# Performance work log

Measured on AMD Instinct MI355X. Metric: run time of the kernel, lower is better.

## Reference

```python
import jax, jax.numpy as jnp
from jax import lax
import numpy as np

GB_MAX = 3      # BandEst guard-band upper bound
RB = 1          # refer_band
PAD = RB + 1    # refer_band + init_guard_band(1)
N_OFF = 16      # ring offsets: kernel (4,4) -> N=16
BN_EPS = 1e-5

def _ring_offsets():
    idx = np.arange(-PAD, PAD + 1)
    X, Y = np.meshgrid(idx, idx, indexing='ij')
    hp = wp = 2 * PAD + 1
    def ring(M):
        return np.concatenate([M[0:RB, 0:wp - RB].ravel(), M[0:hp - RB, wp - RB:wp].ravel(),
                               M[hp - RB:hp, RB:wp].ravel(), M[RB:hp, 0:RB].ravel()])
    return ring(X).astype(np.float32), ring(Y).astype(np.float32)

PRF_X, PRF_Y = _ring_offsets()
BLOCK = np.repeat(np.arange(4), N_OFF // 4)  # offset n -> direction block (top,right,bottom,left)


def q_shift(x, H, W, shift=1, gamma=0.25):
    B, T, C = x.shape
    img = x.transpose(0, 2, 1).reshape(B, C, H, W)
    g = int(C * gamma)
    out = jnp.zeros_like(img)
    out = out.at[:, 0:g, :, shift:].set(img[:, 0:g, :, :W - shift])
    out = out.at[:, g:2 * g, :, :W - shift].set(img[:, g:2 * g, :, shift:])
    out = out.at[:, 2 * g:3 * g, shift:, :].set(img[:, 2 * g:3 * g, :H - shift, :])
    out = out.at[:, 3 * g:4 * g, :H - shift, :].set(img[:, 3 * g:4 * g, shift:, :])
    out = out.at[:, 4 * g:].set(img[:, 4 * g:])
    return out.reshape(B, C, T).transpose(0, 2, 1)


def bi_wkv(w, u, k, v):
    # Bi-directional WKV: y_t = (sum_{i<t} e^{-(t-1-i)w + k_i} v_i + e^{u+k_t} v_t
    #                            + sum_{i>t} e^{-(i-1-t)w + k_i} v_i) / (same with v->1)
    B, T, C = k.shape
    kT = k.transpose(1, 0, 2)
    vT = v.transpose(1, 0, 2)

    def step(carry, kv):
        m, a, b = carry  # state represents e^m * (a, b): (sum exp, weighted v)
        kt, vt = kv
        out = (m, a, b)  # exclusive prefix (excludes current token)
        m2 = jnp.maximum(m - w, kt)
        e1 = jnp.exp(m - w - m2)
        e2 = jnp.exp(kt - m2)
        return (m2, e1 * a + e2, e1 * b + e2 * vt), out

    init = (jnp.full((B, C), -1e38, k.dtype), jnp.zeros((B, C), k.dtype), jnp.zeros((B, C), k.dtype))
    _, (mf, af, bf) = lax.scan(step, init, (kT, vT))
    _, (mb, ab, bb) = lax.scan(step, init, (kT[::-1], vT[::-1]))
    mb, ab, bb = mb[::-1], ab[::-1], bb[::-1]
    ms = u + kT
    M = jnp.maximum(jnp.maximum(mf, mb), ms)
    ef, eb, es = jnp.exp(mf - M), jnp.exp(mb - M), jnp.exp(ms - M)
    num = ef * bf + eb * bb + es * vT
    den = ef * af + eb * ab + es
    return (num / den).transpose(1, 0, 2)


def band_est(x, cvw, cvb, bns_v, bnb_v, chw, chb, bns_h, bnb_h):
    dn = ('NCHW', 'OIHW', 'NCHW')
    gv = lax.conv_general_dilated(x, cvw, (1, 1), ((GB_MAX, GB_MAX), (0, 0)), dimension_numbers=dn) + cvb[None, :, None, None]
    gh = lax.conv_general_dilated(x, chw, (1, 1), ((0, 0), (GB_MAX, GB_MAX)), dimension_numbers=dn) + chb[None, :, None, None]
    inv = np.float32(1.0 / np.sqrt(1.0 + BN_EPS))  # eval BN: running mean 0, var 1
    gv = gv * (bns_v * inv)[None, :, None, None] + bnb_v[None, :, None, None]
    gh = gh * (bns_h * inv)[None, :, None, None] + bnb_h[None, :, None, None]
    return jnp.concatenate([jax.nn.sigmoid(gv), jax.nn.sigmoid(gh)], 1) * (GB_MAX - 1)


def _gather(xp_flat, ix, iy, wp, h, w):
    b, c = xp_flat.shape[0], xp_flat.shape[1]
    idx = (ix * wp + iy).reshape(b, 1, -1)
    return jnp.take_along_axis(xp_flat, idx, axis=2).reshape(b, c, h, w, N_OFF)


def ada_peak(x_img, cvw, cvb, bns_v, bnb_v, chw, chb, bns_h, bnb_h):
    b, c, h, w = x_img.shape
    xp = jnp.pad(x_img, ((0, 0), (0, 0), (PAD, PAD), (PAD, PAD)), mode='edge')
    hp, wp = h + 2 * PAD, w + 2 * PAD
    xp_flat = xp.reshape(b, c, hp * wp)
    gb = band_est(x_img, cvw, cvb, bns_v, bnb_v, chw, chb, bns_h, bnb_h)  # (b,4,h,w)
    zero = jnp.zeros_like(gb[:, 0])
    mvx = jnp.stack([-gb[:, 0], zero, gb[:, 1], zero], -1)  # (b,h,w,4) per block
    mvy = jnp.stack([zero, gb[:, 3], zero, -gb[:, 2]], -1)
    move_x = mvx[..., BLOCK]  # (b,h,w,16)
    move_y = mvy[..., BLOCK]
    cx = jnp.arange(PAD, h + PAD, dtype=x_img.dtype)
    cy = jnp.arange(PAD, w + PAD, dtype=x_img.dtype)
    px = cx[None, :, None, None] + jnp.asarray(PRF_X)[None, None, None, :] + move_x
    py = cy[None, None, :, None] + jnp.asarray(PRF_Y)[None, None, None, :] + move_y
    flx = jnp.floor(lax.stop_gradient(px))
    fly = jnp.floor(lax.stop_gradient(py))
    q_lt_x = jnp.clip(flx, 0, hp - 1)
    q_lt_y = jnp.clip(fly, 0, wp - 1)
    q_rb_x = jnp.clip(flx + 1, 0, hp - 1)
    q_rb_y = jnp.clip(fly + 1, 0, wp - 1)
    pxc = jnp.clip(px, 0, hp - 1)
    pyc = jnp.clip(py, 0, wp - 1)
    g_lt = (1 + (q_lt_x - pxc)) * (1 + (q_lt_y - pyc))
    g_rb = (1 - (q_rb_x - pxc)) * (1 - (q_rb_y - pyc))
    x_lt = _gather(xp_flat, q_lt_x.astype(jnp.int32), q_lt_y.astype(jnp.int32), wp, h, w)
    x_rb = _gather(xp_flat, q_rb_x.astype(jnp.int32), q_rb_y.astype(jnp.int32), wp, h, w)
    x_r = g_lt[:, None] * x_lt + g_rb[:, None] * x_rb
    return x_img[..., None] - x_r  # (b,c,h,w,N): center-minus-reference peak feature


def setup_inputs():
    key = jax.random.key(0)
    B, H, W, C = 2, 64, 64, 192
    ks = jax.random.split(key, 16)
    s = 0.02
    return {
        'x': jax.random.normal(ks[0], (B, H * W, C), jnp.float32),
        'h': H, 'w': W,
        'mix_k': jax.random.uniform(ks[1], (1, 1, C), jnp.float32),
        'mix_v': jax.random.uniform(ks[2], (1, 1, C), jnp.float32),
        'mix_r': jax.random.uniform(ks[3], (1, 1, C), jnp.float32),
        'Wk': jax.random.normal(ks[4], (C, C), jnp.float32) * s,
        'Wv': jax.random.normal(ks[5], (C, C), jnp.float32) * s,
        'Wr': jax.random.normal(ks[6], (C, C), jnp.float32) * s,
        'Wo': jax.random.normal(ks[7], (C, C), jnp.float32) * s,
        'spatial_decay': jax.random.normal(ks[8], (C,), jnp.float32),
        'spatial_first': jax.random.normal(ks[9], (C,), jnp.float32),
        'cvw': jax.random.normal(ks[10], (2, C, 2 * GB_MAX + 1, 1), jnp.float32) * s,
        'cvb': jnp.zeros((2,), jnp.float32),
        'bns_v': jnp.ones((2,), jnp.float32),
        'bnb_v': jnp.zeros((2,), jnp.float32),
        'chw': jax.random.normal(ks[11], (2, C, 1, 2 * GB_MAX + 1), jnp.float32) * s,
        'chb': jnp.zeros((2,), jnp.float32),
        'bns_h': jnp.ones((2,), jnp.float32),
        'bnb_h': jnp.zeros((2,), jnp.float32),
    }


def reference(x, h, w, mix_k, mix_v, mix_r, Wk, Wv, Wr, Wo, spatial_decay, spatial_first,
              cvw, cvb, bns_v, bnb_v, chw, chb, bns_h, bnb_h):
    B, T, C = x.shape
    xx = q_shift(x, h, w)
    xk = x * mix_k + xx * (1 - mix_k)
    xv = x * mix_v + xx * (1 - mix_v)
    xr = x * mix_r + xx * (1 - mix_r)
    k = xk @ Wk
    v = xv @ Wv
    sr = jax.nn.sigmoid(xr @ Wr)
    # deformable peak branch (AdaPeak2D) on the token grid, pooled over the N=16 ring samples
    x_img = x.transpose(0, 2, 1).reshape(B, C, h, w)
    peak = ada_peak(x_img, cvw, cvb, bns_v, bnb_v, chw, chb, bns_h, bnb_h).mean(-1)
    v = v + peak.reshape(B, C, T).transpose(0, 2, 1)
    y = bi_wkv(spatial_decay / T, spatial_first / T, k, v)
    return (sr * y) @ Wo
```

## Files before the change

kernel.cpp:

```cpp
#include <hip/hip_runtime.h>
#include <hip/hip_bf16.h>

#define BATCH 2
#define TLEN 4096
#define CC 192
#define PADC 2
#define APAD 40
#define WPAD 265

typedef __attribute__((ext_vector_type(8))) short bf16x8;
typedef __attribute__((ext_vector_type(4))) float f32x4;

__device__ __constant__ float PRF_X[16] = {-2,-2,-2,-2, -2,-1,0,1, 2,2,2,2, -1,0,1,2};
__device__ __constant__ float PRF_Y[16] = {-2,-1,0,1, 2,2,2,2, -1,0,1,2, -2,-2,-2,-2};

__device__ __forceinline__ unsigned short f2bf(float f) {
    unsigned u = __float_as_uint(f);
    u = (u + 0x7FFF + ((u >> 16) & 1)) >> 16;
    return (unsigned short)u;
}
__device__ __forceinline__ float bf2f(unsigned short h) {
    return __uint_as_float(((unsigned)h) << 16);
}

__global__ __launch_bounds__(256) void k_split_x(const float* __restrict__ x,
                                                 unsigned short* __restrict__ XH,
                                                 unsigned short* __restrict__ XL,
                                                 unsigned short* __restrict__ ZP) {
    if (blockIdx.x == 0 && threadIdx.x < 32) ZP[threadIdx.x] = 0;
    int idx = blockIdx.x * 256 + threadIdx.x;
    float4 v = *(const float4*)(x + (size_t)idx * 4);
    ushort4 hh, ll;
    float f, fh;
    f = v.x; hh.x = f2bf(f); fh = bf2f(hh.x); ll.x = f2bf(f - fh);
    f = v.y; hh.y = f2bf(f); fh = bf2f(hh.y); ll.y = f2bf(f - fh);
    f = v.z; hh.z = f2bf(f); fh = bf2f(hh.z); ll.z = f2bf(f - fh);
    f = v.w; hh.w = f2bf(f); fh = bf2f(hh.w); ll.w = f2bf(f - fh);
    *(ushort4*)(XH + (size_t)idx * 4) = hh;
    *(ushort4*)(XL + (size_t)idx * 4) = ll;
}

__global__ __launch_bounds__(256) void k_wcat_t(const float* __restrict__ Wk,
                                                const float* __restrict__ Wv,
                                                const float* __restrict__ Wr,
                                                const float* __restrict__ mk,
                                                const float* __restrict__ mv,
                                                const float* __restrict__ mr,
                                                unsigned short* __restrict__ WTH,
                                                unsigned short* __restrict__ WTL) {
    int idx = blockIdx.x * 256 + threadIdx.x;
    int n = idx / 384, k = idx - n * 384;
    int sec = n / CC, nc = n - sec * CC;
    const float* W   = (sec == 0) ? Wk : (sec == 1) ? Wv : Wr;
    const float* mix = (sec == 0) ? mk : (sec == 1) ? mv : mr;
    float wv = (k < CC) ? mix[k] * W[k * CC + nc]
                        : (1.0f - mix[k - CC]) * W[(k - CC) * CC + nc];
    unsigned short h = f2bf(wv);
    WTH[idx] = h;
    WTL[idx] = f2bf(wv - bf2f(h));
}

__global__ __launch_bounds__(256) void k_prep_wo(const float* __restrict__ Wo,
                                                 unsigned short* __restrict__ WoTH,
                                                 unsigned short* __restrict__ WoTL) {
    int idx = blockIdx.x * 256 + threadIdx.x;
    int n = idx / CC, k = idx - n * CC;
    float wv = Wo[k * CC + n];
    unsigned short h = f2bf(wv);
    WoTH[idx] = h;
    WoTL[idx] = f2bf(wv - bf2f(h));
}

__global__ __launch_bounds__(128, 2) void k_gemm1_mfma(
        const unsigned short* __restrict__ XH, const unsigned short* __restrict__ XL,
        const unsigned short* __restrict__ WTH, const unsigned short* __restrict__ WTL,
        const unsigned short* __restrict__ ZP,
        float* __restrict__ ZTk, float* __restrict__ Zv, float* __restrict__ ZTr) {
    __shared__ __align__(16) char smem[34816];
    unsigned short* sAh = (unsigned short*)(smem);
    unsigned short* sAl = (unsigned short*)(smem + 10240);
    unsigned short* sBh = (unsigned short*)(smem + 20480);
    unsigned short* sBl = (unsigned short*)(smem + 25600);

    const int tid  = threadIdx.x;
    const int w    = tid >> 6;
    const int lane = tid & 63;
    const int bx = blockIdx.x;
    const int bm = blockIdx.y * 128;
    const int bn = bx * 64;
    const int lc  = tid & 3;
    const int ar0 = tid >> 2;

    f32x4 acc[4][4];
#pragma unroll
    for (int i = 0; i < 4; ++i)
#pragma unroll
        for (int j = 0; j < 4; ++j) acc[i][j] = f32x4{0.f, 0.f, 0.f, 0.f};

    uint4 rA[8], rB[4];

    auto loadA = [&](int step) {
        int k0 = step * 32;
#pragma unroll
        for (int q = 0; q < 4; ++q) {
            int rg = bm + ar0 + q * 32;
            const unsigned short *srcH, *srcL;
            if (k0 < CC) {
                size_t o = (size_t)rg * CC + k0 + lc * 8;
                srcH = XH + o; srcL = XL + o;
            } else {
                int c = k0 - CC + lc * 8;
                int g = c / 48;
                int t = rg & (TLEN - 1);
                int ri = t >> 6, rj = t & 63;
                int dr; bool ok;
                if      (g == 0) { dr = -1;  ok = (rj > 0);  }
                else if (g == 1) { dr =  1;  ok = (rj < 63); }
                else if (g == 2) { dr = -64; ok = (ri > 0);  }
                else             { dr =  64; ok = (ri < 63); }
                if (ok) { size_t o = (size_t)(rg + dr) * CC + c; srcH = XH + o; srcL = XL + o; }
                else    { srcH = ZP; srcL = ZP; }
            }
            rA[q * 2]     = *(const uint4*)srcH;
            rA[q * 2 + 1] = *(const uint4*)srcL;
        }
    };
    auto loadB = [&](int step) {
        int k0 = step * 32;
#pragma unroll
        for (int q = 0; q < 2; ++q) {
            size_t o = (size_t)(bn + ar0 + q * 32) * 384 + k0 + lc * 8;
            rB[q * 2]     = *(const uint4*)(WTH + o);
            rB[q * 2 + 1] = *(const uint4*)(WTL + o);
        }
    };
    auto writeS = [&]() {
#pragma unroll
        for (int q = 0; q < 4; ++q) {
            int off = (ar0 + q * 32) * APAD + lc * 8;
            *(uint4*)&sAh[off] = rA[q * 2];
            *(uint4*)&sAl[off] = rA[q * 2 + 1];
        }
#pragma unroll
        for (int q = 0; q < 2; ++q) {
            int off = (ar0 + q * 32) * APAD + lc * 8;
            *(uint4*)&sBh[off] = rB[q * 2];
            *(uint4*)&sBl[off] = rB[q * 2 + 1];
        }
    };

    const int r15 = lane & 15, ksub = lane >> 4;
    const int pc8 = ksub * 8;

    loadA(0); loadB(0);
    for (int step = 0; step < 12; ++step) {
        __syncthreads();
        writeS();
        __syncthreads();
        if (step < 11) { loadA(step + 1); loadB(step + 1); }
        bf16x8 ah[4], al[4], bh[4], bl[4];
#pragma unroll
        for (int f = 0; f < 4; ++f) {
            int ra = (w * 64 + f * 16 + r15) * APAD + pc8;
            ah[f] = *(const bf16x8*)&sAh[ra];
            al[f] = *(const bf16x8*)&sAl[ra];
            int rb = (f * 16 + r15) * APAD + pc8;
            bh[f] = *(const bf16x8*)&sBh[rb];
            bl[f] = *(const bf16x8*)&sBl[rb];
        }
#pragma unroll
        for (int fr = 0; fr < 4; ++fr)
#pragma unroll
            for (int fc = 0; fc < 4; ++fc) {
                acc[fr][fc] = __builtin_amdgcn_mfma_f32_16x16x32_bf16(ah[fr], bh[fc], acc[fr][fc], 0, 0, 0);
                acc[fr][fc] = __builtin_amdgcn_mfma_f32_16x16x32_bf16(ah[fr], bl[fc], acc[fr][fc], 0, 0, 0);
                acc[fr][fc] = __builtin_amdgcn_mfma_f32_16x16x32_bf16(al[fr], bh[fc], acc[fr][fc], 0, 0, 0);
            }
    }

    __syncthreads();
    float* T = (float*)smem + w * (64 * 68);
    const int sec   = bx / 3;
    const int cbase = (bx - sec * 3) * 64;

    if (sec == 1) {
#pragma unroll
        for (int fr = 0; fr < 4; ++fr)
#pragma unroll
            for (int fc = 0; fc < 4; ++fc) {
                int r0 = fr * 16 + ksub * 4, c = fc * 16 + r15;
                f32x4 v = acc[fr][fc];
                T[(r0 + 0) * 68 + c] = v[0];
                T[(r0 + 1) * 68 + c] = v[1];
                T[(r0 + 2) * 68 + c] = v[2];
                T[(r0 + 3) * 68 + c] = v[3];
            }
        __syncthreads();
#pragma unroll
        for (int it = 0; it < 16; ++it) {
            int row = it * 4 + ksub;
            float4 o = *(const float4*)&T[row * 68 + r15 * 4];
            *(float4*)(Zv + (size_t)(bm + w * 64 + row) * CC + cbase + r15 * 4) = o;
        }
    } else {
        float* D = (sec == 0) ? ZTk : ZTr;
#pragma unroll
        for (int fr = 0; fr < 4; ++fr)
#pragma unroll
            for (int fc = 0; fc < 4; ++fc) {
                int r0 = fr * 16 + ksub * 4, c = fc * 16 + r15;
                *(f32x4*)&T[c * 68 + r0] = acc[fr][fc];
            }
        __syncthreads();
#pragma unroll
        for (int cg = 0; cg < 16; ++cg) {
            int c = cg * 4 + ksub;
            float4 o = *(const float4*)&T[c * 68 + r15 * 4];
            *(float4*)(D + (size_t)(cbase + c) * 8192 + bm + w * 64 + r15 * 4) = o;
        }
    }
}

__global__ __launch_bounds__(128, 2) void k_gemm2_mfma(
        const unsigned short* __restrict__ PH, const unsigned short* __restrict__ PL,
        const unsigned short* __restrict__ WoTH, const unsigned short* __restrict__ WoTL,
        float* __restrict__ out) {
    __shared__ __align__(16) char smem[34816];
    unsigned short* sAh = (unsigned short*)(smem);
    unsigned short* sAl = (unsigned short*)(smem + 10240);
    unsigned short* sBh = (unsigned short*)(smem + 20480);
    unsigned short* sBl = (unsigned short*)(smem + 25600);

    const int tid  = threadIdx.x;
    const int w    = tid >> 6;
    const int lane = tid & 63;
    const int bn = blockIdx.x * 64;
    const int bm = blockIdx.y * 128;
    const int lc  = tid & 3;
    const int ar0 = tid >> 2;

    f32x4 acc[4][4];
#pragma unroll
    for (int i = 0; i < 4; ++i)
#pragma unroll
        for (int j = 0; j < 4; ++j) acc[i][j] = f32x4{0.f, 0.f, 0.f, 0.f};

    uint4 rA[8], rB[4];
    auto loadAB = [&](int step) {
        int k0 = step * 32;
#pragma unroll
        for (int q = 0; q < 4; ++q) {
            size_t o = (size_t)(bm + ar0 + q * 32) * CC + k0 + lc * 8;
            rA[q * 2]     = *(const uint4*)(PH + o);
            rA[q * 2 + 1] = *(const uint4*)(PL + o);
        }
#pragma unroll
        for (int q = 0; q < 2; ++q) {
            size_t o = (size_t)(bn + ar0 + q * 32) * CC + k0 + lc * 8;
            rB[q * 2]     = *(const uint4*)(WoTH + o);
            rB[q * 2 + 1] = *(const uint4*)(WoTL + o);
        }
    };
    auto writeS = [&]() {
#pragma unroll
        for (int q = 0; q < 4; ++q) {
            int off = (ar0 + q * 32) * APAD + lc * 8;
            *(uint4*)&sAh[off] = rA[q * 2];
            *(uint4*)&sAl[off] = rA[q * 2 + 1];
        }
#pragma unroll
        for (int q = 0; q < 2; ++q) {
            int off = (ar0 + q * 32) * APAD + lc * 8;
            *(uint4*)&sBh[off] = rB[q * 2];
            *(uint4*)&sBl[off] = rB[q * 2 + 1];
        }
    };

    const int r15 = lane & 15, ksub = lane >> 4;
    const int pc8 = ksub * 8;

    loadAB(0);
    for (int step = 0; step < 6; ++step) {
        __syncthreads();
        writeS();
        __syncthreads();
        if (step < 5) loadAB(step + 1);
        bf16x8 ah[4], al[4], bh[4], bl[4];
#pragma unroll
        for (int f = 0; f < 4; ++f) {
            int ra = (w * 64 + f * 16 + r15) * APAD + pc8;
            ah[f] = *(const bf16x8*)&sAh[ra];
            al[f] = *(const bf16x8*)&sAl[ra];
            int rb = (f * 16 + r15) * APAD + pc8;
            bh[f] = *(const bf16x8*)&sBh[rb];
            bl[f] = *(const bf16x8*)&sBl[rb];
        }
#pragma unroll
        for (int fr = 0; fr < 4; ++fr)
#pragma unroll
            for (int fc = 0; fc < 4; ++fc) {
                acc[fr][fc] = __builtin_amdgcn_mfma_f32_16x16x32_bf16(ah[fr], bh[fc], acc[fr][fc], 0, 0, 0);
                acc[fr][fc] = __builtin_amdgcn_mfma_f32_16x16x32_bf16(ah[fr], bl[fc], acc[fr][fc], 0, 0, 0);
                acc[fr][fc] = __builtin_amdgcn_mfma_f32_16x16x32_bf16(al[fr], bh[fc], acc[fr][fc], 0, 0, 0);
            }
    }

    __syncthreads();
    float* T = (float*)smem + w * (64 * 68);
#pragma unroll
    for (int fr = 0; fr < 4; ++fr)
#pragma unroll
        for (int fc = 0; fc < 4; ++fc) {
            int r0 = fr * 16 + ksub * 4, c = fc * 16 + r15;
            f32x4 v = acc[fr][fc];
            T[(r0 + 0) * 68 + c] = v[0];
            T[(r0 + 1) * 68 + c] = v[1];
            T[(r0 + 2) * 68 + c] = v[2];
            T[(r0 + 3) * 68 + c] = v[3];
        }
    __syncthreads();
#pragma unroll
    for (int it = 0; it < 16; ++it) {
        int row = it * 4 + ksub;
        float4 o = *(const float4*)&T[row * 68 + r15 * 4];
        *(float4*)(out + (size_t)(bm + w * 64 + row) * CC + bn + r15 * 4) = o;
    }
}

__global__ __launch_bounds__(192) void k_bandpeak(const float* __restrict__ x,
                                                  const float* __restrict__ cvw,
                                                  const float* __restrict__ cvb,
                                                  const float* __restrict__ bns_v,
                                                  const float* __restrict__ bnb_v,
                                                  const float* __restrict__ chw,
                                                  const float* __restrict__ chb,
                                                  const float* __restrict__ bns_h,
                                                  const float* __restrict__ bnb_h,
                                                  float* __restrict__ Zv) {
    int pixg = blockIdx.x;
    int b   = pixg >> 12;
    int pix = pixg & 4095;
    int i = pix >> 6, j = pix & 63;
    int c = threadIdx.x;
    size_t xbase = (size_t)b * TLEN * CC;

    float sv0 = 0.f, sv1 = 0.f, sh0 = 0.f, sh1 = 0.f;
#pragma unroll
    for (int t = 0; t < 7; ++t) {
        int ii = i + t - 3;
        if (ii >= 0 && ii < 64) {
            float xv = x[xbase + (size_t)(ii * 64 + j) * CC + c];
            sv0 = fmaf(xv, cvw[(0 * CC + c) * 7 + t], sv0);
            sv1 = fmaf(xv, cvw[(1 * CC + c) * 7 + t], sv1);
        }
        int jj = j + t - 3;
        if (jj >= 0 && jj < 64) {
            float xh = x[xbase + (size_t)(i * 64 + jj) * CC + c];
            sh0 = fmaf(xh, chw[(0 * CC + c) * 7 + t], sh0);
            sh1 = fmaf(xh, chw[(1 * CC + c) * 7 + t], sh1);
        }
    }
    __shared__ float red[4][CC];
    __shared__ float gsh[4];
    red[0][c] = sv0; red[1][c] = sv1; red[2][c] = sh0; red[3][c] = sh1;
    __syncthreads();
    if (c < 64) {
#pragma unroll
        for (int r = 0; r < 4; ++r) {
            float v = red[r][c] + red[r][c + 64] + red[r][c + 128];
            v += __shfl_xor(v, 32);
            v += __shfl_xor(v, 16);
            v += __shfl_xor(v, 8);
            v += __shfl_xor(v, 4);
            v += __shfl_xor(v, 2);
            v += __shfl_xor(v, 1);
            if (c == 0) {
                const float inv = 0.9999950000374997f;
                float bias, sc, sh;
                if (r < 2) { bias = cvb[r];     sc = bns_v[r];     sh = bnb_v[r]; }
                else       { bias = chb[r - 2]; sc = bns_h[r - 2]; sh = bnb_h[r - 2]; }
                float g = (v + bias) * (sc * inv) + sh;
                gsh[r] = 2.0f / (1.0f + expf(-g));
            }
        }
    }
    __syncthreads();

    __shared__ int   l_lt[16], l_rb[16];
    __shared__ float l_glt[16], l_grb[16];
    if (c < 16) {
        int n = c, blk = n >> 2;
        float mx = (blk == 0) ? -gsh[0] : (blk == 2) ? gsh[1] : 0.0f;
        float my = (blk == 1) ?  gsh[3] : (blk == 3) ? -gsh[2] : 0.0f;
        float px = (float)(i + PADC) + PRF_X[n] + mx;
        float py = (float)(j + PADC) + PRF_Y[n] + my;
        float flx = floorf(px), fly = floorf(py);
        float qltx = fminf(fmaxf(flx, 0.f), 67.f);
        float qlty = fminf(fmaxf(fly, 0.f), 67.f);
        float qrbx = fminf(fmaxf(flx + 1.f, 0.f), 67.f);
        float qrby = fminf(fmaxf(fly + 1.f, 0.f), 67.f);
        float pxc = fminf(fmaxf(px, 0.f), 67.f);
        float pyc = fminf(fmaxf(py, 0.f), 67.f);
        float glt = (1.f + (qltx - pxc)) * (1.f + (qlty - pyc));
        float grb = (1.f - (qrbx - pxc)) * (1.f - (qrby - pyc));
        int sltx = min(max((int)qltx - PADC, 0), 63);
        int slty = min(max((int)qlty - PADC, 0), 63);
        int srbx = min(max((int)qrbx - PADC, 0), 63);
        int srby = min(max((int)qrby - PADC, 0), 63);
        l_lt[n] = sltx * 64 + slty;
        l_rb[n] = srbx * 64 + srby;
        l_glt[n] = glt;
        l_grb[n] = grb;
    }
    __syncthreads();

    float acc = 0.f;
#pragma unroll
    for (int n = 0; n < 16; ++n) {
        acc = fmaf(l_glt[n], x[xbase + (size_t)l_lt[n] * CC + c], acc);
        acc = fmaf(l_grb[n], x[xbase + (size_t)l_rb[n] * CC + c], acc);
    }
    float peak = x[xbase + (size_t)pix * CC + c] - acc * 0.0625f;
    Zv[((size_t)b * TLEN + pix) * CC + c] += peak;
}

__global__ __launch_bounds__(256) void k_transv(const float* __restrict__ Zv,
                                                float* __restrict__ ZTv) {
    __shared__ float tile[64][65];
    int tid = threadIdx.x;
    int rb = (blockIdx.x & 127) * 64;
    int cb = (blockIdx.x >> 7) * 64;
    int tr  = tid >> 4;
    int tc4 = (tid & 15) * 4;
#pragma unroll
    for (int q = 0; q < 4; ++q) {
        int r = tr + q * 16;
        float4 v = *(const float4*)(Zv + (size_t)(rb + r) * CC + cb + tc4);
        *(float4*)&tile[r][tc4] = v;
    }
    __syncthreads();
#pragma unroll
    for (int q = 0; q < 4; ++q) {
        int ccol = tr + q * 16;
        float4 o = {tile[tc4 + 0][ccol], tile[tc4 + 1][ccol],
                    tile[tc4 + 2][ccol], tile[tc4 + 3][ccol]};
        *(float4*)(ZTv + (size_t)(cb + ccol) * 8192 + rb + tc4) = o;
    }
}

__global__ __launch_bounds__(256) void k_transP(const float* __restrict__ PT,
                                                unsigned short* __restrict__ PH,
                                                unsigned short* __restrict__ PL) {
    __shared__ float tile[64][65];
    int tid = threadIdx.x;
    int mb = (blockIdx.x & 127) * 64;
    int cb = (blockIdx.x >> 7) * 64;
    int tr  = tid >> 4;
    int tc4 = (tid & 15) * 4;
#pragma unroll
    for (int q = 0; q < 4; ++q) {
        int cr = tr + q * 16;
        float4 v = *(const float4*)(PT + (size_t)(cb + cr) * 8192 + mb + tc4);
        *(float4*)&tile[cr][tc4] = v;
    }
    __syncthreads();
#pragma unroll
    for (int q = 0; q < 4; ++q) {
        int m = tr + q * 16;
        ushort4 hh, ll;
        float f, fh;
        f = tile[tc4 + 0][m]; hh.x = f2bf(f); fh = bf2f(hh.x); ll.x = f2bf(f - fh);
        f = tile[tc4 + 1][m]; hh.y = f2bf(f); fh = bf2f(hh.y); ll.y = f2bf(f - fh);
        f = tile[tc4 + 2][m]; hh.z = f2bf(f); fh = bf2f(hh.z); ll.z = f2bf(f - fh);
        f = tile[tc4 + 3][m]; hh.w = f2bf(f); fh = bf2f(hh.w); ll.w = f2bf(f - fh);
        size_t o = (size_t)(mb + m) * CC + cb + tc4;
        *(ushort4*)(PH + o) = hh;
        *(ushort4*)(PL + o) = ll;
    }
}

__global__ __launch_bounds__(256) void k_wkv2(const float* __restrict__ ZT,
                                              float* __restrict__ PT,
                                              const float* __restrict__ sd,
                                              const float* __restrict__ sf) {
    const int NTH = 256, CH = 16;
    int c = blockIdx.x % CC;
    int b = blockIdx.x / CC;
    const float w = sd[c] * (1.0f / 4096.0f);
    const float u = sf[c] * (1.0f / 4096.0f);

    __shared__ float buf[16 * WPAD];
    __shared__ float s_m[NTH], s_a[NTH], s_b[NTH], s_L[NTH];

    int tid = threadIdx.x;
    size_t base = (size_t)c * 8192 + (size_t)b * TLEN;

    float kr[CH], vr[CH], rr[CH];

    auto coopLoad = [&](const float* src) {
#pragma unroll
        for (int i = 0; i < 4; ++i) {
            int g = i * 1024 + tid * 4;
            float4 v = *(const float4*)(src + g);
            int jj0 = g & 15;
            int tp  = g >> 4;
            buf[(jj0 + 0) * WPAD + tp] = v.x;
            buf[(jj0 + 1) * WPAD + tp] = v.y;
            buf[(jj0 + 2) * WPAD + tp] = v.z;
            buf[(jj0 + 3) * WPAD + tp] = v.w;
        }
    };
    auto chunkRead = [&](float* dst) {
#pragma unroll
        for (int jj = 0; jj < CH; ++jj) dst[jj] = buf[jj * WPAD + tid];
    };

    coopLoad(ZT + base);                                __syncthreads();
    chunkRead(kr);                                      __syncthreads();
    coopLoad(ZT + (size_t)CC * 8192 + base);            __syncthreads();
    chunkRead(vr);                                      __syncthreads();
    coopLoad(ZT + (size_t)2 * CC * 8192 + base);        __syncthreads();
    chunkRead(rr);                                      __syncthreads();

    float m = -1e38f, a = 0.f, bb = 0.f;
#pragma unroll
    for (int jj = 0; jj < CH; ++jj) {
        float kt = kr[jj], vt = vr[jj];
        float m2 = fmaxf(m - w, kt);
        float e1 = expf(m - w - m2);
        float e2 = expf(kt - m2);
        a = e1 * a + e2;
        bb = e1 * bb + e2 * vt;
        m = m2;
    }
    s_m[tid] = m; s_a[tid] = a; s_b[tid] = bb; s_L[tid] = (float)CH;
    float L = (float)CH;
    for (int d = 1; d < NTH; d <<= 1) {
        __syncthreads();
        float pm = 0, pa = 0, pb = 0, pL = 0;
        bool has = (tid >= d);
        if (has) { pm = s_m[tid - d]; pa = s_a[tid - d]; pb = s_b[tid - d]; pL = s_L[tid - d]; }
        __syncthreads();
        if (has) {
            float pdec = pm - L * w;
            float m2 = fmaxf(pdec, m);
            float e1 = expf(pdec - m2);
            float e2 = expf(m - m2);
            a  = e1 * pa + e2 * a;
            bb = e1 * pb + e2 * bb;
            m = m2; L += pL;
            s_m[tid] = m; s_a[tid] = a; s_b[tid] = bb; s_L[tid] = L;
        }
    }
    __syncthreads();
    float fm = -1e38f, fa = 0.f, fb = 0.f;
    if (tid > 0) { fm = s_m[tid - 1]; fa = s_a[tid - 1]; fb = s_b[tid - 1]; }
    __syncthreads();

    m = -1e38f; a = 0.f; bb = 0.f;
#pragma unroll
    for (int jj = CH - 1; jj >= 0; --jj) {
        float kt = kr[jj], vt = vr[jj];
        float m2 = fmaxf(m - w, kt);
        float e1 = expf(m - w - m2);
        float e2 = expf(kt - m2);
        a = e1 * a + e2;
        bb = e1 * bb + e2 * vt;
        m = m2;
    }
    s_m[tid] = m; s_a[tid] = a; s_b[tid] = bb; s_L[tid] = (float)CH;
    L = (float)CH;
    for (int d = 1; d < NTH; d <<= 1) {
        __syncthreads();
        float pm = 0, pa = 0, pb = 0, pL = 0;
        bool has = (tid + d) < NTH;
        if (has) { pm = s_m[tid + d]; pa = s_a[tid + d]; pb = s_b[tid + d]; pL = s_L[tid + d]; }
        __syncthreads();
        if (has) {
            float pdec = pm - L * w;
            float m2 = fmaxf(m, pdec);
            float e1 = expf(m - m2);
            float e2 = expf(pdec - m2);
            a  = e1 * a + e2 * pa;
            bb = e1 * bb + e2 * pb;
            m = m2; L += pL;
            s_m[tid] = m; s_a[tid] = a; s_b[tid] = bb; s_L[tid] = L;
        }
    }
    __syncthreads();
    float bm = -1e38f, ba = 0.f, bbv = 0.f;
    if (tid < NTH - 1) { bm = s_m[tid + 1]; ba = s_a[tid + 1]; bbv = s_b[tid + 1]; }
    __syncthreads();

    float em[CH], ea[CH], eb[CH];
    m = bm; a = ba; bb = bbv;
#pragma unroll
    for (int jj = CH - 1; jj >= 0; --jj) {
        em[jj] = m; ea[jj] = a; eb[jj] = bb;
        float kt = kr[jj], vt = vr[jj];
        float m2 = fmaxf(m - w, kt);
        float e1 = expf(m - w - m2);
        float e2 = expf(kt - m2);
        a = e1 * a + e2;
        bb = e1 * bb + e2 * vt;
        m = m2;
    }

    m = fm; a = fa; bb = fb;
#pragma unroll
    for (int jj = 0; jj < CH; ++jj) {
        float kt = kr[jj], vt = vr[jj];
        float ms = u + kt;
        float M = fmaxf(fmaxf(m, em[jj]), ms);
        float ef  = expf(m - M);
        float ebk = expf(em[jj] - M);
        float es  = expf(ms - M);
        float num = ef * bb + ebk * eb[jj] + es * vt;
        float den = ef * a + ebk * ea[jj] + es;
        float y = num / den;
        float sr = 1.0f / (1.0f + expf(-rr[jj]));
        buf[jj * WPAD + tid] = sr * y;
        float m2 = fmaxf(m - w, kt);
        float e1 = expf(m - w - m2);
        float e2 = expf(kt - m2);
        a = e1 * a + e2;
        bb = e1 * bb + e2 * vt;
        m = m2;
    }
    __syncthreads();
#pragma unroll
    for (int i = 0; i < 4; ++i) {
        int g = i * 1024 + tid * 4;
        int jj0 = g & 15;
        int tp  = g >> 4;
        float4 o = {buf[(jj0 + 0) * WPAD + tp], buf[(jj0 + 1) * WPAD + tp],
                    buf[(jj0 + 2) * WPAD + tp], buf[(jj0 + 3) * WPAD + tp]};
        *(float4*)(PT + base + g) = o;
    }
}

extern "C" void kernel_launch(void* const* d_in, const int* in_sizes, int n_in,
                              void* d_out, int out_size, void* d_ws, size_t ws_size,
                              hipStream_t stream) {
    const float* x     = (const float*)d_in[0];
    const float* mix_k = (const float*)d_in[3];
    const float* mix_v = (const float*)d_in[4];
    const float* mix_r = (const float*)d_in[5];
    const float* Wk    = (const float*)d_in[6];
    const float* Wv    = (const float*)d_in[7];
    const float* Wr    = (const float*)d_in[8];
    const float* Wo    = (const float*)d_in[9];
    const float* sd    = (const float*)d_in[10];
    const float* sf    = (const float*)d_in[11];
    const float* cvw   = (const float*)d_in[12];
    const float* cvb   = (const float*)d_in[13];
    const float* bns_v = (const float*)d_in[14];
    const float* bnb_v = (const float*)d_in[15];
    const float* chw   = (const float*)d_in[16];
    const float* chb   = (const float*)d_in[17];
    const float* bns_h = (const float*)d_in[18];
    const float* bnb_h = (const float*)d_in[19];
    float* out = (float*)d_out;
    char* W = (char*)d_ws;

    float*          Zv   = (float*)(W + 0);
    float*          ZTk  = (float*)(W + 6291456);
    float*          ZTv  = (float*)(W + 12582912);
    float*          ZTr  = (float*)(W + 18874368);
    unsigned short* XH   = (unsigned short*)(W + 12582912);
    unsigned short* XL   = (unsigned short*)(W + 15728640);
    unsigned short* PH   = (unsigned short*)(W + 6291456);
    unsigned short* PL   = (unsigned short*)(W + 9437184);
    float*          PT   = Zv;
    unsigned short* WTH  = (unsigned short*)(W + 25165824);
    unsigned short* WTL  = (unsigned short*)(W + 25608192);
    unsigned short* WoTH = (unsigned short*)(W + 26050560);
    unsigned short* WoTL = (unsigned short*)(W + 26124288);
    unsigned short* ZP   = (unsigned short*)(W + 26198016);

    k_split_x<<<1536, 256, 0, stream>>>(x, XH, XL, ZP);
    k_wcat_t<<<864, 256, 0, stream>>>(Wk, Wv, Wr, mix_k, mix_v, mix_r, WTH, WTL);
    k_prep_wo<<<144, 256, 0, stream>>>(Wo, WoTH, WoTL);
    k_gemm1_mfma<<<dim3(9, 64), 128, 0, stream>>>(XH, XL, WTH, WTL, ZP, ZTk, Zv, ZTr);
    k_bandpeak<<<8192, 192, 0, stream>>>(x, cvw, cvb, bns_v, bnb_v, chw, chb, bns_h, bnb_h, Zv);
    k_transv<<<384, 256, 0, stream>>>(Zv, ZTv);
    k_wkv2<<<384, 256, 0, stream>>>(ZTk, PT, sd, sf);
    k_transP<<<384, 256, 0, stream>>>(PT, PH, PL);
    k_gemm2_mfma<<<dim3(3, 64), 128, 0, stream>>>(PH, PL, WoTH, WoTL, out);
}
```

Measured before the change: 264.7 us.

## Fuse bf16 hi/lo splitting into both GEMMs and drop split/transpose kernels

Removes the k_split_x and k_transP kernels. Both GEMMs now read fp32 activations directly and convert them to bf16 hi/lo pairs while staging into shared memory. gemm2 reads the transposed PT layout and transposes it through scalar LDS stores. The GEMM tiles are retuned (64-row tiles, 256 threads, gemm1 covering a full 192-column section per block), and the LDS-staged epilogue is replaced by direct global stores. This saves two launches and their intermediate memory traffic, at the cost of more conversion work per block, uncoalesced scalar stores for Zv/out, and bank-conflicting scalar LDS writes.

```diff
diff --git a/kernel.cpp b/kernel.cpp
--- a/kernel.cpp
+++ b/kernel.cpp
@@ -21,23 +21,6 @@
 }
 __device__ __forceinline__ float bf2f(unsigned short h) {
     return __uint_as_float(((unsigned)h) << 16);
-}
-
-__global__ __launch_bounds__(256) void k_split_x(const float* __restrict__ x,
-                                                 unsigned short* __restrict__ XH,
-                                                 unsigned short* __restrict__ XL,
-                                                 unsigned short* __restrict__ ZP) {
-    if (blockIdx.x == 0 && threadIdx.x < 32) ZP[threadIdx.x] = 0;
-    int idx = blockIdx.x * 256 + threadIdx.x;
-    float4 v = *(const float4*)(x + (size_t)idx * 4);
-    ushort4 hh, ll;
-    float f, fh;
-    f = v.x; hh.x = f2bf(f); fh = bf2f(hh.x); ll.x = f2bf(f - fh);
-    f = v.y; hh.y = f2bf(f); fh = bf2f(hh.y); ll.y = f2bf(f - fh);
-    f = v.z; hh.z = f2bf(f); fh = bf2f(hh.z); ll.z = f2bf(f - fh);
-    f = v.w; hh.w = f2bf(f); fh = bf2f(hh.w); ll.w = f2bf(f - fh);
-    *(ushort4*)(XH + (size_t)idx * 4) = hh;
-    *(ushort4*)(XL + (size_t)idx * 4) = ll;
 }
 
 __global__ __launch_bounds__(256) void k_wcat_t(const float* __restrict__ Wk,
@@ -71,84 +54,85 @@
     WoTL[idx] = f2bf(wv - bf2f(h));
 }
 
-__global__ __launch_bounds__(128, 2) void k_gemm1_mfma(
-        const unsigned short* __restrict__ XH, const unsigned short* __restrict__ XL,
+__global__ __launch_bounds__(256, 2) void k_gemm1_mfma(
+        const float* __restrict__ x,
         const unsigned short* __restrict__ WTH, const unsigned short* __restrict__ WTL,
-        const unsigned short* __restrict__ ZP,
         float* __restrict__ ZTk, float* __restrict__ Zv, float* __restrict__ ZTr) {
-    __shared__ __align__(16) char smem[34816];
-    unsigned short* sAh = (unsigned short*)(smem);
-    unsigned short* sAl = (unsigned short*)(smem + 10240);
-    unsigned short* sBh = (unsigned short*)(smem + 20480);
-    unsigned short* sBl = (unsigned short*)(smem + 25600);
-
+    __shared__ unsigned short sAh[64 * APAD], sAl[64 * APAD];
+    __shared__ unsigned short sBh[192 * APAD], sBl[192 * APAD];
     const int tid  = threadIdx.x;
     const int w    = tid >> 6;
     const int lane = tid & 63;
-    const int bx = blockIdx.x;
-    const int bm = blockIdx.y * 128;
-    const int bn = bx * 64;
-    const int lc  = tid & 3;
-    const int ar0 = tid >> 2;
-
-    f32x4 acc[4][4];
-#pragma unroll
-    for (int i = 0; i < 4; ++i)
-#pragma unroll
-        for (int j = 0; j < 4; ++j) acc[i][j] = f32x4{0.f, 0.f, 0.f, 0.f};
-
-    uint4 rA[8], rB[4];
-
-    auto loadA = [&](int step) {
-        int k0 = step * 32;
-#pragma unroll
-        for (int q = 0; q < 4; ++q) {
-            int rg = bm + ar0 + q * 32;
-            const unsigned short *srcH, *srcL;
-            if (k0 < CC) {
-                size_t o = (size_t)rg * CC + k0 + lc * 8;
-                srcH = XH + o; srcL = XL + o;
-            } else {
-                int c = k0 - CC + lc * 8;
-                int g = c / 48;
-                int t = rg & (TLEN - 1);
-                int ri = t >> 6, rj = t & 63;
-                int dr; bool ok;
-                if      (g == 0) { dr = -1;  ok = (rj > 0);  }
-                else if (g == 1) { dr =  1;  ok = (rj < 63); }
-                else if (g == 2) { dr = -64; ok = (ri > 0);  }
-                else             { dr =  64; ok = (ri < 63); }
-                if (ok) { size_t o = (size_t)(rg + dr) * CC + c; srcH = XH + o; srcL = XL + o; }
-                else    { srcH = ZP; srcL = ZP; }
-            }
-            rA[q * 2]     = *(const uint4*)srcH;
-            rA[q * 2 + 1] = *(const uint4*)srcL;
-        }
+    const int sec  = blockIdx.x;
+    const int bm   = blockIdx.y * 64;
+
+    const int arow = tid >> 2;
+    const int akc  = (tid & 3) * 8;
+    const int rg   = bm + arow;
+    const int t    = rg & (TLEN - 1);
+    const int ri   = t >> 6, rj = t & 63;
+
+    f32x4 acc[2][6];
+#pragma unroll
+    for (int i = 0; i < 2; ++i)
+#pragma unroll
+        for (int j = 0; j < 6; ++j) acc[i][j] = f32x4{0.f, 0.f, 0.f, 0.f};
+
+    float4 fA0, fA1;
+    uint4 rB[6];
+
+    auto loadA = [&](int k0) {
+        bool aok;
+        const float* src;
+        if (k0 < CC) {
+            src = x + (size_t)rg * CC + k0 + akc;
+            aok = true;
+        } else {
+            int c = k0 - CC + akc;
+            int g = c / 48;
+            int dr;
+            if      (g == 0) { dr = -1;  aok = (rj > 0);  }
+            else if (g == 1) { dr =  1;  aok = (rj < 63); }
+            else if (g == 2) { dr = -64; aok = (ri > 0);  }
+            else             { dr =  64; aok = (ri < 63); }
+            src = x + (size_t)(rg + dr) * CC + c;
+        }
+        if (aok) { fA0 = *(const float4*)src; fA1 = *(const float4*)(src + 4); }
+        else     { fA0 = make_float4(0.f,0.f,0.f,0.f); fA1 = fA0; }
     };
-    auto loadB = [&](int step) {
-        int k0 = step * 32;
-#pragma unroll
-        for (int q = 0; q < 2; ++q) {
-            size_t o = (size_t)(bn + ar0 + q * 32) * 384 + k0 + lc * 8;
+    auto loadB = [&](int k0) {
+#pragma unroll
+        for (int q = 0; q < 3; ++q) {
+            int ch  = q * 256 + tid;
+            int col = ch >> 2, kc = (ch & 3) * 8;
+            size_t o = (size_t)(sec * CC + col) * 384 + k0 + kc;
             rB[q * 2]     = *(const uint4*)(WTH + o);
             rB[q * 2 + 1] = *(const uint4*)(WTL + o);
         }
     };
     auto writeS = [&]() {
-#pragma unroll
-        for (int q = 0; q < 4; ++q) {
-            int off = (ar0 + q * 32) * APAD + lc * 8;
-            *(uint4*)&sAh[off] = rA[q * 2];
-            *(uint4*)&sAl[off] = rA[q * 2 + 1];
-        }
-#pragma unroll
-        for (int q = 0; q < 2; ++q) {
-            int off = (ar0 + q * 32) * APAD + lc * 8;
-            *(uint4*)&sBh[off] = rB[q * 2];
-            *(uint4*)&sBl[off] = rB[q * 2 + 1];
+        float fa[8] = {fA0.x, fA0.y, fA0.z, fA0.w, fA1.x, fA1.y, fA1.z, fA1.w};
+        unsigned hu[4], lu[4];
+#pragma unroll
+        for (int j = 0; j < 4; ++j) {
+            unsigned short h0 = f2bf(fa[2*j]),   l0 = f2bf(fa[2*j]   - bf2f(h0));
+            unsigned short h1 = f2bf(fa[2*j+1]), l1 = f2bf(fa[2*j+1] - bf2f(h1));
+            hu[j] = (unsigned)h0 | ((unsigned)h1 << 16);
+            lu[j] = (unsigned)l0 | ((unsigned)l1 << 16);
+        }
+        *(uint4*)&sAh[arow * APAD + akc] = make_uint4(hu[0], hu[1], hu[2], hu[3]);
+        *(uint4*)&sAl[arow * APAD + akc] = make_uint4(lu[0], lu[1], lu[2], lu[3]);
+#pragma unroll
+        for (int q = 0; q < 3; ++q) {
+            int ch  = q * 256 + tid;
+            int col = ch >> 2, kc = (ch & 3) * 8;
+            *(uint4*)&sBh[col * APAD + kc] = rB[q * 2];
+            *(uint4*)&sBl[col * APAD + kc] = rB[q * 2 + 1];
         }
     };
 
+    const int wrb = (w >> 1) * 32;
+    const int wcb = (w & 1) * 96;
     const int r15 = lane & 15, ksub = lane >> 4;
     const int pc8 = ksub * 8;
 
@@ -157,125 +141,103 @@
         __syncthreads();
         writeS();
         __syncthreads();
-        if (step < 11) { loadA(step + 1); loadB(step + 1); }
-        bf16x8 ah[4], al[4], bh[4], bl[4];
-#pragma unroll
-        for (int f = 0; f < 4; ++f) {
-            int ra = (w * 64 + f * 16 + r15) * APAD + pc8;
+        if (step < 11) { loadA((step + 1) * 32); loadB((step + 1) * 32); }
+        bf16x8 ah[2], al[2], bh[6], bl[6];
+#pragma unroll
+        for (int f = 0; f < 2; ++f) {
+            int ra = (wrb + f * 16 + r15) * APAD + pc8;
             ah[f] = *(const bf16x8*)&sAh[ra];
             al[f] = *(const bf16x8*)&sAl[ra];
-            int rb = (f * 16 + r15) * APAD + pc8;
+        }
+#pragma unroll
+        for (int f = 0; f < 6; ++f) {
+            int rb = (wcb + f * 16 + r15) * APAD + pc8;
             bh[f] = *(const bf16x8*)&sBh[rb];
             bl[f] = *(const bf16x8*)&sBl[rb];
         }
 #pragma unroll
-        for (int fr = 0; fr < 4; ++fr)
-#pragma unroll
-            for (int fc = 0; fc < 4; ++fc) {
+        for (int fr = 0; fr < 2; ++fr)
+#pragma unroll
+            for (int fc = 0; fc < 6; ++fc) {
                 acc[fr][fc] = __builtin_amdgcn_mfma_f32_16x16x32_bf16(ah[fr], bh[fc], acc[fr][fc], 0, 0, 0);
                 acc[fr][fc] = __builtin_amdgcn_mfma_f32_16x16x32_bf16(ah[fr], bl[fc], acc[fr][fc], 0, 0, 0);
                 acc[fr][fc] = __builtin_amdgcn_mfma_f32_16x16x32_bf16(al[fr], bh[fc], acc[fr][fc], 0, 0, 0);
             }
     }
 
-    __syncthreads();
-    float* T = (float*)smem + w * (64 * 68);
-    const int sec   = bx / 3;
-    const int cbase = (bx - sec * 3) * 64;
-
     if (sec == 1) {
 #pragma unroll
-        for (int fr = 0; fr < 4; ++fr)
-#pragma unroll
-            for (int fc = 0; fc < 4; ++fc) {
-                int r0 = fr * 16 + ksub * 4, c = fc * 16 + r15;
+        for (int fr = 0; fr < 2; ++fr)
+#pragma unroll
+            for (int fc = 0; fc < 6; ++fc) {
+                int m0  = wrb + fr * 16 + ksub * 4;
+                int col = wcb + fc * 16 + r15;
                 f32x4 v = acc[fr][fc];
-                T[(r0 + 0) * 68 + c] = v[0];
-                T[(r0 + 1) * 68 + c] = v[1];
-                T[(r0 + 2) * 68 + c] = v[2];
-                T[(r0 + 3) * 68 + c] = v[3];
+#pragma unroll
+                for (int q = 0; q < 4; ++q)
+                    Zv[(size_t)(bm + m0 + q) * CC + col] = v[q];
             }
-        __syncthreads();
-#pragma unroll
-        for (int it = 0; it < 16; ++it) {
-            int row = it * 4 + ksub;
-            float4 o = *(const float4*)&T[row * 68 + r15 * 4];
-            *(float4*)(Zv + (size_t)(bm + w * 64 + row) * CC + cbase + r15 * 4) = o;
-        }
     } else {
         float* D = (sec == 0) ? ZTk : ZTr;
 #pragma unroll
-        for (int fr = 0; fr < 4; ++fr)
-#pragma unroll
-            for (int fc = 0; fc < 4; ++fc) {
-                int r0 = fr * 16 + ksub * 4, c = fc * 16 + r15;
-                *(f32x4*)&T[c * 68 + r0] = acc[fr][fc];
+        for (int fr = 0; fr < 2; ++fr)
+#pragma unroll
+            for (int fc = 0; fc < 6; ++fc) {
+                int m0  = wrb + fr * 16 + ksub * 4;
+                int col = wcb + fc * 16 + r15;
+                f32x4 v = acc[fr][fc];
+                *(float4*)(D + (size_t)col * 8192 + bm + m0) = make_float4(v[0], v[1], v[2], v[3]);
             }
-        __syncthreads();
-#pragma unroll
-        for (int cg = 0; cg < 16; ++cg) {
-            int c = cg * 4 + ksub;
-            float4 o = *(const float4*)&T[c * 68 + r15 * 4];
-            *(float4*)(D + (size_t)(cbase + c) * 8192 + bm + w * 64 + r15 * 4) = o;
-        }
-    }
-}
-
-__global__ __launch_bounds__(128, 2) void k_gemm2_mfma(
-        const unsigned short* __restrict__ PH, const unsigned short* __restrict__ PL,
+    }
+}
+
+__global__ __launch_bounds__(256, 2) void k_gemm2_mfma(
+        const float* __restrict__ PT,
         const unsigned short* __restrict__ WoTH, const unsigned short* __restrict__ WoTL,
         float* __restrict__ out) {
-    __shared__ __align__(16) char smem[34816];
-    unsigned short* sAh = (unsigned short*)(smem);
-    unsigned short* sAl = (unsigned short*)(smem + 10240);
-    unsigned short* sBh = (unsigned short*)(smem + 20480);
-    unsigned short* sBl = (unsigned short*)(smem + 25600);
-
+    __shared__ unsigned short sAh[64 * APAD], sAl[64 * APAD];
+    __shared__ unsigned short sBh[64 * APAD], sBl[64 * APAD];
     const int tid  = threadIdx.x;
     const int w    = tid >> 6;
     const int lane = tid & 63;
-    const int bn = blockIdx.x * 64;
-    const int bm = blockIdx.y * 128;
-    const int lc  = tid & 3;
-    const int ar0 = tid >> 2;
-
-    f32x4 acc[4][4];
-#pragma unroll
-    for (int i = 0; i < 4; ++i)
-#pragma unroll
-        for (int j = 0; j < 4; ++j) acc[i][j] = f32x4{0.f, 0.f, 0.f, 0.f};
-
-    uint4 rA[8], rB[4];
-    auto loadAB = [&](int step) {
-        int k0 = step * 32;
-#pragma unroll
-        for (int q = 0; q < 4; ++q) {
-            size_t o = (size_t)(bm + ar0 + q * 32) * CC + k0 + lc * 8;
-            rA[q * 2]     = *(const uint4*)(PH + o);
-            rA[q * 2 + 1] = *(const uint4*)(PL + o);
-        }
-#pragma unroll
-        for (int q = 0; q < 2; ++q) {
-            size_t o = (size_t)(bn + ar0 + q * 32) * CC + k0 + lc * 8;
-            rB[q * 2]     = *(const uint4*)(WoTH + o);
-            rB[q * 2 + 1] = *(const uint4*)(WoTL + o);
-        }
+    const int bn   = blockIdx.x * 64;
+    const int bm   = blockIdx.y * 64;
+
+    const int akk = tid >> 3;
+    const int am8 = (tid & 7) * 8;
+    const int bcol = tid >> 2;
+    const int bkc  = (tid & 3) * 8;
+
+    f32x4 acc[2][2];
+#pragma unroll
+    for (int i = 0; i < 2; ++i)
+#pragma unroll
+        for (int j = 0; j < 2; ++j) acc[i][j] = f32x4{0.f, 0.f, 0.f, 0.f};
+
+    float4 p0, p1;
+    uint4 rbh, rbl;
+    auto loadAB = [&](int k0) {
+        const float* pa = PT + (size_t)(k0 + akk) * 8192 + bm + am8;
+        p0 = *(const float4*)pa;
+        p1 = *(const float4*)(pa + 4);
+        size_t o = (size_t)(bn + bcol) * CC + k0 + bkc;
+        rbh = *(const uint4*)(WoTH + o);
+        rbl = *(const uint4*)(WoTL + o);
     };
     auto writeS = [&]() {
-#pragma unroll
-        for (int q = 0; q < 4; ++q) {
-            int off = (ar0 + q * 32) * APAD + lc * 8;
-            *(uint4*)&sAh[off] = rA[q * 2];
-            *(uint4*)&sAl[off] = rA[q * 2 + 1];
-        }
-#pragma unroll
-        for (int q = 0; q < 2; ++q) {
-            int off = (ar0 + q * 32) * APAD + lc * 8;
-            *(uint4*)&sBh[off] = rB[q * 2];
-            *(uint4*)&sBl[off] = rB[q * 2 + 1];
-        }
+        float fa[8] = {p0.x, p0.y, p0.z, p0.w, p1.x, p1.y, p1.z, p1.w};
+#pragma unroll
+        for (int j = 0; j < 8; ++j) {
+            unsigned short h = f2bf(fa[j]);
+            sAh[(am8 + j) * APAD + akk] = h;
+            sAl[(am8 + j) * APAD + akk] = f2bf(fa[j] - bf2f(h));
+        }
+        *(uint4*)&sBh[bcol * APAD + bkc] = rbh;
+        *(uint4*)&sBl[bcol * APAD + bkc] = rbl;
     };
 
+    const int wrb = (w >> 1) * 32;
+    const int wcb = (w & 1) * 32;
     const int r15 = lane & 15, ksub = lane >> 4;
     const int pc8 = ksub * 8;
 
@@ -284,47 +246,38 @@
         __syncthreads();
         writeS();
         __syncthreads();
-        if (step < 5) loadAB(step + 1);
-        bf16x8 ah[4], al[4], bh[4], bl[4];
-#pragma unroll
-        for (int f = 0; f < 4; ++f) {
-            int ra = (w * 64 + f * 16 + r15) * APAD + pc8;
+        if (step < 5) loadAB((step + 1) * 32);
+        bf16x8 ah[2], al[2], bh[2], bl[2];
+#pragma unroll
+        for (int f = 0; f < 2; ++f) {
+            int ra = (wrb + f * 16 + r15) * APAD + pc8;
             ah[f] = *(const bf16x8*)&sAh[ra];
             al[f] = *(const bf16x8*)&sAl[ra];
-            int rb = (f * 16 + r15) * APAD + pc8;
+            int rb = (wcb + f * 16 + r15) * APAD + pc8;
             bh[f] = *(const bf16x8*)&sBh[rb];
             bl[f] = *(const bf16x8*)&sBl[rb];
         }
 #pragma unroll
-        for (int fr = 0; fr < 4; ++fr)
-#pragma unroll
-            for (int fc = 0; fc < 4; ++fc) {
+        for (int fr = 0; fr < 2; ++fr)
+#pragma unroll
+            for (int fc = 0; fc < 2; ++fc) {
                 acc[fr][fc] = __builtin_amdgcn_mfma_f32_16x16x32_bf16(ah[fr], bh[fc], acc[fr][fc], 0, 0, 0);
                 acc[fr][fc] = __builtin_amdgcn_mfma_f32_16x16x32_bf16(ah[fr], bl[fc], acc[fr][fc], 0, 0, 0);
                 acc[fr][fc] = __builtin_amdgcn_mfma_f32_16x16x32_bf16(al[fr], bh[fc], acc[fr][fc], 0, 0, 0);
             }
     }
 
-    __syncthreads();
-    float* T = (float*)smem + w * (64 * 68);
-#pragma unroll
-    for (int fr = 0; fr < 4; ++fr)
-#pragma unroll
-        for (int fc = 0; fc < 4; ++fc) {
-            int r0 = fr * 16 + ksub * 4, c = fc * 16 + r15;
+#pragma unroll
+    for (int fr = 0; fr < 2; ++fr)
+#pragma unroll
+        for (int fc = 0; fc < 2; ++fc) {
+            int m0  = wrb + fr * 16 + ksub * 4;
+            int col = bn + wcb + fc * 16 + r15;
             f32x4 v = acc[fr][fc];
-            T[(r0 + 0) * 68 + c] = v[0];
-            T[(r0 + 1) * 68 + c] = v[1];
-            T[(r0 + 2) * 68 + c] = v[2];
-            T[(r0 + 3) * 68 + c] = v[3];
-        }
-    __syncthreads();
-#pragma unroll
-    for (int it = 0; it < 16; ++it) {
-        int row = it * 4 + ksub;
-        float4 o = *(const float4*)&T[row * 68 + r15 * 4];
-        *(float4*)(out + (size_t)(bm + w * 64 + row) * CC + bn + r15 * 4) = o;
-    }
+#pragma unroll
+            for (int q = 0; q < 4; ++q)
+                out[(size_t)(bm + m0 + q) * CC + col] = v[q];
+        }
 }
 
 __global__ __launch_bounds__(192) void k_bandpeak(const float* __restrict__ x,
@@ -448,37 +401,6 @@
     }
 }
 
-__global__ __launch_bounds__(256) void k_transP(const float* __restrict__ PT,
-                                                unsigned short* __restrict__ PH,
-                                                unsigned short* __restrict__ PL) {
-    __shared__ float tile[64][65];
-    int tid = threadIdx.x;
-    int mb = (blockIdx.x & 127) * 64;
-    int cb = (blockIdx.x >> 7) * 64;
-    int tr  = tid >> 4;
-    int tc4 = (tid & 15) * 4;
-#pragma unroll
-    for (int q = 0; q < 4; ++q) {
-        int cr = tr + q * 16;
-        float4 v = *(const float4*)(PT + (size_t)(cb + cr) * 8192 + mb + tc4);
-        *(float4*)&tile[cr][tc4] = v;
-    }
-    __syncthreads();
-#pragma unroll
-    for (int q = 0; q < 4; ++q) {
-        int m = tr + q * 16;
-        ushort4 hh, ll;
-        float f, fh;
-        f = tile[tc4 + 0][m]; hh.x = f2bf(f); fh = bf2f(hh.x); ll.x = f2bf(f - fh);
-        f = tile[tc4 + 1][m]; hh.y = f2bf(f); fh = bf2f(hh.y); ll.y = f2bf(f - fh);
-        f = tile[tc4 + 2][m]; hh.z = f2bf(f); fh = bf2f(hh.z); ll.z = f2bf(f - fh);
-        f = tile[tc4 + 3][m]; hh.w = f2bf(f); fh = bf2f(hh.w); ll.w = f2bf(f - fh);
-        size_t o = (size_t)(mb + m) * CC + cb + tc4;
-        *(ushort4*)(PH + o) = hh;
-        *(ushort4*)(PL + o) = ll;
-    }
-}
-
 __global__ __launch_bounds__(256) void k_wkv2(const float* __restrict__ ZT,
                                               float* __restrict__ PT,
                                               const float* __restrict__ sd,
@@ -588,12 +510,12 @@
         }
     }
     __syncthreads();
-    float bm = -1e38f, ba = 0.f, bbv = 0.f;
-    if (tid < NTH - 1) { bm = s_m[tid + 1]; ba = s_a[tid + 1]; bbv = s_b[tid + 1]; }
+    float bm2 = -1e38f, ba = 0.f, bbv = 0.f;
+    if (tid < NTH - 1) { bm2 = s_m[tid + 1]; ba = s_a[tid + 1]; bbv = s_b[tid + 1]; }
     __syncthreads();
 
     float em[CH], ea[CH], eb[CH];
-    m = bm; a = ba; bb = bbv;
+    m = bm2; a = ba; bb = bbv;
 #pragma unroll
     for (int jj = CH - 1; jj >= 0; --jj) {
         em[jj] = m; ea[jj] = a; eb[jj] = bb;
@@ -667,24 +589,17 @@
     float*          ZTk  = (float*)(W + 6291456);
     float*          ZTv  = (float*)(W + 12582912);
     float*          ZTr  = (float*)(W + 18874368);
-    unsigned short* XH   = (unsigned short*)(W + 12582912);
-    unsigned short* XL   = (unsigned short*)(W + 15728640);
-    unsigned short* PH   = (unsigned short*)(W + 6291456);
-    unsigned short* PL   = (unsigned short*)(W + 9437184);
     float*          PT   = Zv;
     unsigned short* WTH  = (unsigned short*)(W + 25165824);
     unsigned short* WTL  = (unsigned short*)(W + 25608192);
     unsigned short* WoTH = (unsigned short*)(W + 26050560);
     unsigned short* WoTL = (unsigned short*)(W + 26124288);
-    unsigned short* ZP   = (unsigned short*)(W + 26198016);
-
-    k_split_x<<<1536, 256, 0, stream>>>(x, XH, XL, ZP);
+
     k_wcat_t<<<864, 256, 0, stream>>>(Wk, Wv, Wr, mix_k, mix_v, mix_r, WTH, WTL);
     k_prep_wo<<<144, 256, 0, stream>>>(Wo, WoTH, WoTL);
-    k_gemm1_mfma<<<dim3(9, 64), 128, 0, stream>>>(XH, XL, WTH, WTL, ZP, ZTk, Zv, ZTr);
+    k_gemm1_mfma<<<dim3(3, 128), 256, 0, stream>>>(x, WTH, WTL, ZTk, Zv, ZTr);
     k_bandpeak<<<8192, 192, 0, stream>>>(x, cvw, cvb, bns_v, bnb_v, chw, chb, bns_h, bnb_h, Zv);
     k_transv<<<384, 256, 0, stream>>>(Zv, ZTv);
     k_wkv2<<<384, 256, 0, stream>>>(ZTk, PT, sd, sf);
-    k_transP<<<384, 256, 0, stream>>>(PT, PH, PL);
-    k_gemm2_mfma<<<dim3(3, 64), 128, 0, stream>>>(PH, PL, WoTH, WoTL, out);
-}
+    k_gemm2_mfma<<<dim3(3, 128), 256, 0, stream>>>(PT, WoTH, WoTL, out);
+}
```

New measurement: 234.1 us. 11.5% less time.
